# Optimization experiments

Hardware: AMD Instinct MI355X
Metric: run time of the kernel (lower is better)

Reference implementation:

```python
import jax, jax.numpy as jnp
import numpy as np
from jax import lax

# pywt db4 reconstruction low-pass (scaling) coefficients
_REC_LO = np.array([
    0.23037781330885523, 0.7148465705525415, 0.6308807679295904,
    -0.02798376941698385, -0.18703481171888114, 0.030841381835986965,
    0.032883011666982945, -0.010597401784997278], dtype=np.float64)
_DEC_LO = _REC_LO[::-1].copy()                       # pywt dec_lo = reversed rec_lo
_DEC_HI = (_REC_LO * ((-1.0) ** (np.arange(8) + 1)))  # pywt qmf: dec_hi[k] = (-1)^(k+1) rec_lo[k]
FLEN = 8
LEVEL = 4


def _dwt_level(x):
    """One pywt dwt level, mode='symmetric'. x: [N, n] -> (cA, cD) each [N, floor((n+7)/2)]."""
    # half-sample symmetric extension by FLEN-1 on each side, then drop the first
    # sample so a stride-2 VALID conv lands on pywt's odd-indexed outputs.
    ext = jnp.pad(x, ((0, 0), (FLEN - 1, FLEN - 1)), mode='symmetric')[:, 1:]
    # pywt performs true convolution with dec filters -> flip kernels for XLA correlation
    k = jnp.stack([_DEC_LO[::-1], _DEC_HI[::-1]]).astype(x.dtype)[:, None, :]  # [2,1,8]
    y = lax.conv_general_dilated(ext[:, None, :], k, window_strides=(2,),
                                 padding='VALID',
                                 dimension_numbers=('NCH', 'OIH', 'NCH'))  # [N,2,out]
    return y[:, 0], y[:, 1]


def setup_inputs() -> dict:
    key = jax.random.key(0)
    x = jax.random.normal(key, (64, 32, 8192), dtype=jnp.float32)
    return {"x": x}


def reference(x) -> jnp.ndarray:
    """Batched pywt.wavedec(x, 'db4', mode='symmetric', level=4), coeffs concatenated.
    x: [B, C, L] -> [B, C, wavelet_len] with order [cA4, cD4, cD3, cD2, cD1]."""
    B, C, L = x.shape
    a = x.reshape(B * C, L)
    details = []
    for _ in range(LEVEL):
        a, d = _dwt_level(a)
        details.append(d)
    coeffs = jnp.concatenate([a] + details[::-1], axis=-1)  # [B*C, total]
    return coeffs.reshape(B, C, -1)
```

## Files before the change

### kernel.cpp

```cpp
#include <hip/hip_runtime.h>

#define NT 256

constexpr int L0 = 8192;
constexpr int N1 = 4099;
constexpr int N2 = 2053;
constexpr int N3 = 1030;
constexpr int N4 = 518;
constexpr int ROW_OUT = N4 + N4 + N3 + N2 + N1;

constexpr float GLO[8] = {
    0.23037781330885523f,  0.7148465705525415f,   0.6308807679295904f,
   -0.02798376941698385f, -0.18703481171888114f,  0.030841381835986965f,
    0.032883011666982945f, -0.010597401784997278f };
constexpr float GHI[8] = {
   -0.010597401784997278f, -0.032883011666982945f, 0.030841381835986965f,
    0.18703481171888114f,  -0.02798376941698385f,  -0.6308807679295904f,
    0.7148465705525415f,   -0.23037781330885523f };

__device__ __forceinline__ void set_pads(float* __restrict__ e, float* __restrict__ o,
                                         int n, int nE, int nO, int nout, int tid)
{
    if (tid < 4) {
        e[-1 - tid] = o[tid];
        o[-1 - tid] = e[tid];
        if (tid < nout - nE) e[nE + tid] = o[n - 1 - nE - tid];
        if (tid < nout - nO) o[nO + tid] = e[n - 1 - nO - tid];
    }
}

template <bool LAST>
__device__ __forceinline__ void dwt_level_vec(const float* __restrict__ e,
                                              const float* __restrict__ o,
                                              int nout,
                                              float* __restrict__ eN,
                                              float* __restrict__ oN,
                                              float* __restrict__ loG,
                                              float* __restrict__ hiG, int tid)
{
    const int nv = nout & ~3;
    const float4* e4 = (const float4*)(e - 4);
    const float4* o4 = (const float4*)(o - 4);
    for (int i0 = 4 * tid; i0 < nv; i0 += 4 * NT) {
        const int q = i0 >> 2;
        float4 eL = e4[q], eH = e4[q + 1];
        float4 oL = o4[q], oH = o4[q + 1];
        float cE[8] = {eL.x, eL.y, eL.z, eL.w, eH.x, eH.y, eH.z, eH.w};
        float cO[8] = {oL.x, oL.y, oL.z, oL.w, oH.x, oH.y, oH.z, oH.w};
        float lo[4], hi[4];
#pragma unroll
        for (int r = 0; r < 4; ++r) {
            float l = 0.f, h = 0.f;
#pragma unroll
            for (int m = 0; m < 4; ++m) {
                float ve = cE[r + 1 + m];
                float vo = cO[r + 1 + m];
                l = fmaf(GLO[2 * m], ve, l);
                l = fmaf(GLO[2 * m + 1], vo, l);
                h = fmaf(GHI[2 * m], ve, h);
                h = fmaf(GHI[2 * m + 1], vo, h);
            }
            lo[r] = l; hi[r] = h;
        }
        hiG[i0 + 0] = hi[0]; hiG[i0 + 1] = hi[1];
        hiG[i0 + 2] = hi[2]; hiG[i0 + 3] = hi[3];
        if (LAST) {
            loG[i0 + 0] = lo[0]; loG[i0 + 1] = lo[1];
            loG[i0 + 2] = lo[2]; loG[i0 + 3] = lo[3];
        } else {
            ((float2*)eN)[q] = make_float2(lo[0], lo[2]);
            ((float2*)oN)[q] = make_float2(lo[1], lo[3]);
        }
    }
    const int rem = nout - nv;
    if (tid < rem) {
        const int i = nv + tid;
        float l = 0.f, h = 0.f;
#pragma unroll
        for (int m = 0; m < 4; ++m) {
            float ve = e[i - 3 + m];
            float vo = o[i - 3 + m];
            l = fmaf(GLO[2 * m], ve, l);
            l = fmaf(GLO[2 * m + 1], vo, l);
            h = fmaf(GHI[2 * m], ve, h);
            h = fmaf(GHI[2 * m + 1], vo, h);
        }
        hiG[i] = h;
        if (LAST) {
            loG[i] = l;
        } else {
            float* t = (i & 1) ? oN : eN;
            t[i >> 1] = l;
        }
    }
}

__global__ __launch_bounds__(NT) void wavedec4_db4(const float* __restrict__ x,
                                                   float* __restrict__ out)
{
    __shared__ __align__(16) float eA[4 + 4096 + 4], oA[4 + 4096 + 4];
    __shared__ __align__(16) float eB[4 + 2050 + 4], oB[4 + 2050 + 4];
    const int tid = threadIdx.x;
    const float* __restrict__ xr = x + blockIdx.x * (size_t)L0;
    float* __restrict__ outr = out + blockIdx.x * (size_t)ROW_OUT;
    float* E0 = eA + 4; float* O0 = oA + 4;
    float* E1 = eB + 4; float* O1 = oB + 4;

    const float4* x4 = (const float4*)xr;
    float2* e2 = (float2*)E0;
    float2* o2 = (float2*)O0;
    for (int idx = tid; idx < L0 / 4; idx += NT) {
        float4 v = x4[idx];
        e2[idx] = make_float2(v.x, v.z);
        o2[idx] = make_float2(v.y, v.w);
    }
    if (tid < 4) {
        E0[-1 - tid] = xr[2 * tid + 1];
        O0[-1 - tid] = xr[2 * tid];
        if (tid < 3) {
            E0[4096 + tid] = xr[8191 - 2 * tid];
            O0[4096 + tid] = xr[8190 - 2 * tid];
        }
    }
    __syncthreads();

    dwt_level_vec<false>(E0, O0, N1, E1, O1, nullptr, outr + (N4 + N4 + N3 + N2), tid);
    __syncthreads();
    set_pads(E1, O1, N1, 2050, 2049, N2, tid);
    __syncthreads();

    dwt_level_vec<false>(E1, O1, N2, E0, O0, nullptr, outr + (N4 + N4 + N3), tid);
    __syncthreads();
    set_pads(E0, O0, N2, 1027, 1026, N3, tid);
    __syncthreads();

    dwt_level_vec<false>(E0, O0, N3, E1, O1, nullptr, outr + (N4 + N4), tid);
    __syncthreads();
    set_pads(E1, O1, N3, 515, 515, N4, tid);
    __syncthreads();

    dwt_level_vec<true>(E1, O1, N4, nullptr, nullptr, outr, outr + N4, tid);
}

extern "C" void kernel_launch(void* const* d_in, const int* in_sizes, int n_in,
                              void* d_out, int out_size, void* d_ws, size_t ws_size,
                              hipStream_t stream) {
    const float* x = (const float*)d_in[0];
    float* out = (float*)d_out;
    const int rows = in_sizes[0] / L0;
    wavedec4_db4<<<dim3(rows), dim3(NT), 0, stream>>>(x, out);
}
```

Measured before the change: 120.5 us.

## Split each row across two blocks with overlapping halo for the 4-level DWT

```diff
diff --git a/kernel.cpp b/kernel.cpp
--- a/kernel.cpp
+++ b/kernel.cpp
@@ -18,33 +18,23 @@
     0.18703481171888114f,  -0.02798376941698385f,  -0.6308807679295904f,
     0.7148465705525415f,   -0.23037781330885523f };
 
-__device__ __forceinline__ void set_pads(float* __restrict__ e, float* __restrict__ o,
-                                         int n, int nE, int nO, int nout, int tid)
+template <bool LAST>
+__device__ __forceinline__ void level_vec(const float* __restrict__ e,
+                                          const float* __restrict__ o,
+                                          int iLo, int iHi,
+                                          float* __restrict__ eN,
+                                          float* __restrict__ oN,
+                                          float* __restrict__ loG,
+                                          float* __restrict__ hiG, int tid)
 {
-    if (tid < 4) {
-        e[-1 - tid] = o[tid];
-        o[-1 - tid] = e[tid];
-        if (tid < nout - nE) e[nE + tid] = o[n - 1 - nE - tid];
-        if (tid < nout - nO) o[nO + tid] = e[n - 1 - nO - tid];
-    }
-}
-
-template <bool LAST>
-__device__ __forceinline__ void dwt_level_vec(const float* __restrict__ e,
-                                              const float* __restrict__ o,
-                                              int nout,
-                                              float* __restrict__ eN,
-                                              float* __restrict__ oN,
-                                              float* __restrict__ loG,
-                                              float* __restrict__ hiG, int tid)
-{
-    const int nv = nout & ~3;
-    const float4* e4 = (const float4*)(e - 4);
-    const float4* o4 = (const float4*)(o - 4);
-    for (int i0 = 4 * tid; i0 < nv; i0 += 4 * NT) {
-        const int q = i0 >> 2;
-        float4 eL = e4[q], eH = e4[q + 1];
-        float4 oL = o4[q], oH = o4[q + 1];
+    const int span = iHi - iLo;
+    const int nv = span & ~3;
+    for (int v = 4 * tid; v < nv; v += 4 * NT) {
+        const int i0 = iLo + v;
+        float4 eL = *(const float4*)(e + i0 - 4);
+        float4 eH = *(const float4*)(e + i0);
+        float4 oL = *(const float4*)(o + i0 - 4);
+        float4 oH = *(const float4*)(o + i0);
         float cE[8] = {eL.x, eL.y, eL.z, eL.w, eH.x, eH.y, eH.z, eH.w};
         float cO[8] = {oL.x, oL.y, oL.z, oL.w, oH.x, oH.y, oH.z, oH.w};
         float lo[4], hi[4];
@@ -68,13 +58,13 @@
             loG[i0 + 0] = lo[0]; loG[i0 + 1] = lo[1];
             loG[i0 + 2] = lo[2]; loG[i0 + 3] = lo[3];
         } else {
-            ((float2*)eN)[q] = make_float2(lo[0], lo[2]);
-            ((float2*)oN)[q] = make_float2(lo[1], lo[3]);
+            *(float2*)(eN + (i0 >> 1)) = make_float2(lo[0], lo[2]);
+            *(float2*)(oN + (i0 >> 1)) = make_float2(lo[1], lo[3]);
         }
     }
-    const int rem = nout - nv;
+    const int rem = span - nv;
     if (tid < rem) {
-        const int i = nv + tid;
+        const int i = iLo + nv + tid;
         float l = 0.f, h = 0.f;
 #pragma unroll
         for (int m = 0; m < 4; ++m) {
@@ -95,51 +85,83 @@
     }
 }
 
-__global__ __launch_bounds__(NT) void wavedec4_db4(const float* __restrict__ x,
-                                                   float* __restrict__ out)
+__global__ __launch_bounds__(NT) void wavedec4_db4_split(const float* __restrict__ x,
+                                                         float* __restrict__ out)
 {
-    __shared__ __align__(16) float eA[4 + 4096 + 4], oA[4 + 4096 + 4];
-    __shared__ __align__(16) float eB[4 + 2050 + 4], oB[4 + 2050 + 4];
+    __shared__ __align__(16) float eA_s[2120], oA_s[2120];
+    __shared__ __align__(16) float eB_s[1068], oB_s[1068];
     const int tid = threadIdx.x;
-    const float* __restrict__ xr = x + blockIdx.x * (size_t)L0;
-    float* __restrict__ outr = out + blockIdx.x * (size_t)ROW_OUT;
-    float* E0 = eA + 4; float* O0 = oA + 4;
-    float* E1 = eB + 4; float* O1 = oB + 4;
+    const int row = blockIdx.x >> 1;
+    const int half = blockIdx.x & 1;
+    const float* __restrict__ xr = x + row * (size_t)L0;
+    float* __restrict__ outr = out + row * (size_t)ROW_OUT;
+    float* cA4 = outr;
+    float* cD4 = outr + N4;
+    float* cD3 = outr + 2 * N4;
+    float* cD2 = outr + 2 * N4 + N3;
+    float* cD1 = outr + 2 * N4 + N3 + N2;
 
-    const float4* x4 = (const float4*)xr;
-    float2* e2 = (float2*)E0;
-    float2* o2 = (float2*)O0;
-    for (int idx = tid; idx < L0 / 4; idx += NT) {
-        float4 v = x4[idx];
-        e2[idx] = make_float2(v.x, v.z);
-        o2[idx] = make_float2(v.y, v.w);
-    }
-    if (tid < 4) {
-        E0[-1 - tid] = xr[2 * tid + 1];
-        O0[-1 - tid] = xr[2 * tid];
-        if (tid < 3) {
+    if (half == 0) {
+        float* E0 = eA_s + 4; float* O0 = oA_s + 4;
+        float* E1 = eB_s + 4; float* O1 = oB_s + 4;
+        const float4* x4 = (const float4*)xr;
+        float2* e2 = (float2*)E0; float2* o2 = (float2*)O0;
+        for (int idx = tid; idx < 4144 / 4; idx += NT) {
+            float4 vv = x4[idx];
+            e2[idx] = make_float2(vv.x, vv.z);
+            o2[idx] = make_float2(vv.y, vv.w);
+        }
+        if (tid < 4) {
+            E0[-1 - tid] = xr[2 * tid + 1];
+            O0[-1 - tid] = xr[2 * tid];
+        }
+        __syncthreads();
+        level_vec<false>(E0, O0, 0, 2072, E1, O1, nullptr, cD1, tid);
+        __syncthreads();
+        if (tid < 4) { E1[-1 - tid] = O1[tid]; O1[-1 - tid] = E1[tid]; }
+        __syncthreads();
+        level_vec<false>(E1, O1, 0, 1036, E0, O0, nullptr, cD2, tid);
+        __syncthreads();
+        if (tid < 4) { E0[-1 - tid] = O0[tid]; O0[-1 - tid] = E0[tid]; }
+        __syncthreads();
+        level_vec<false>(E0, O0, 0, 518, E1, O1, nullptr, cD3, tid);
+        __syncthreads();
+        if (tid < 4) { E1[-1 - tid] = O1[tid]; O1[-1 - tid] = E1[tid]; }
+        __syncthreads();
+        level_vec<true>(E1, O1, 0, 259, nullptr, nullptr, cA4, cD4, tid);
+    } else {
+        float* E0 = eA_s - 1988; float* O0 = oA_s - 1988;
+        float* E1 = eB_s - 996;  float* O1 = oB_s - 996;
+        const float4* x4 = (const float4*)(xr + 3976);
+        float2* e2 = (float2*)eA_s; float2* o2 = (float2*)oA_s;
+        for (int idx = tid; idx < 4216 / 4; idx += NT) {
+            float4 vv = x4[idx];
+            e2[idx] = make_float2(vv.x, vv.z);
+            o2[idx] = make_float2(vv.y, vv.w);
+        }
+        if (tid < 4) {
             E0[4096 + tid] = xr[8191 - 2 * tid];
             O0[4096 + tid] = xr[8190 - 2 * tid];
         }
+        __syncthreads();
+        level_vec<false>(E0, O0, 1992, N1, E1, O1, nullptr, cD1, tid);
+        __syncthreads();
+        if (tid < 3) E1[2050 + tid] = O1[2048 - tid];
+        if (tid < 4) O1[2049 + tid] = E1[2049 - tid];
+        __syncthreads();
+        float* E2 = eA_s - 500; float* O2 = oA_s - 500;
+        level_vec<false>(E1, O1, 1000, N2, E2, O2, nullptr, cD2, tid);
+        __syncthreads();
+        if (tid < 3) E2[1027 + tid] = O2[1025 - tid];
+        if (tid < 4) O2[1026 + tid] = E2[1026 - tid];
+        __syncthreads();
+        float* E3 = eB_s - 252; float* O3 = oB_s - 252;
+        level_vec<false>(E2, O2, 504, N3, E3, O3, nullptr, cD3, tid);
+        __syncthreads();
+        if (tid < 3) { E3[515 + tid] = O3[514 - tid]; O3[515 + tid] = E3[514 - tid]; }
+        __syncthreads();
+        level_vec<true>(E3, O3, 256, N4, nullptr, nullptr, cA4, cD4, tid);
     }
-    __syncthreads();
-
-    dwt_level_vec<false>(E0, O0, N1, E1, O1, nullptr, outr + (N4 + N4 + N3 + N2), tid);
-    __syncthreads();
-    set_pads(E1, O1, N1, 2050, 2049, N2, tid);
-    __syncthreads();
-
-    dwt_level_vec<false>(E1, O1, N2, E0, O0, nullptr, outr + (N4 + N4 + N3), tid);
-    __syncthreads();
-    set_pads(E0, O0, N2, 1027, 1026, N3, tid);
-    __syncthreads();
-
-    dwt_level_vec<false>(E0, O0, N3, E1, O1, nullptr, outr + (N4 + N4), tid);
-    __syncthreads();
-    set_pads(E1, O1, N3, 515, 515, N4, tid);
-    __syncthreads();
-
-    dwt_level_vec<true>(E1, O1, N4, nullptr, nullptr, outr, outr + N4, tid);
 }
 
 extern "C" void kernel_launch(void* const* d_in, const int* in_sizes, int n_in,
@@ -148,5 +170,5 @@
     const float* x = (const float*)d_in[0];
     float* out = (float*)d_out;
     const int rows = in_sizes[0] / L0;
-    wavedec4_db4<<<dim3(rows), dim3(NT), 0, stream>>>(x, out);
+    wavedec4_db4_split<<<dim3(rows * 2), dim3(NT), 0, stream>>>(x, out);
 }
```

Measured after the change: 118.5 us. No clear change (-1.6%).
